# Kernel tuning notes

Hardware: AMD Instinct MI355X
Metric: run time of the kernel (lower is better)

Reference implementation:

```python
import jax, jax.numpy as jnp
import numpy as np
from jax import lax

V, D, P, C = 151936, 1024, 64, 28
B, S = 1, 1024
EPS = 1.1920929e-07  # torch.finfo(float32).eps, used by nn.RMSNorm(eps=None)


def setup_inputs() -> dict:
    key = jax.random.key(0)
    ks = jax.random.split(key, 10)
    return {
        "tokens": jax.random.randint(ks[0], (B, S), 0, V),
        "embed_table": jax.random.normal(ks[1], (V, D), jnp.float32) * 0.02,
        "plane_proj_w": jax.random.normal(ks[2], (C, 2 * P, D), jnp.float32) * (1.0 / np.sqrt(D)),
        "back_proj_w": jax.random.normal(ks[3], (C, D, 2 * P), jnp.float32) * 0.02,
        "base_angles": jax.random.normal(ks[4], (C, P), jnp.float32) * 0.1,
        "angle_gen_w": jax.random.normal(ks[5], (P, D), jnp.float32) * 0.01,
        "scales": jnp.ones((C, D), jnp.float32),
        "shifts": jnp.zeros((C, D), jnp.float32),
        "norm_w": jnp.ones((C, D), jnp.float32),
        "decay_param": jnp.float32(0.9),
        "gate_w": jax.random.normal(ks[6], (D, D), jnp.float32) * 0.02,
        "out_norm_w": jnp.ones((D,), jnp.float32),
        "lm_head_w": jax.random.normal(ks[7], (V, D), jnp.float32) * 0.02,
    }


def _rms_norm(v, w):
    return v * lax.rsqrt(jnp.mean(v * v, axis=-1, keepdims=True) + EPS) * w


def _causal_mix(x, decay_param, gate_w):
    # state_t = d*state_{t-1} + (1-d)*x_t, causal EMA over sequence
    d = jax.nn.sigmoid(decay_param)
    def step(s, xt):
        s = d * s + (1.0 - d) * xt
        return s, s
    _, ys = lax.scan(step, jnp.zeros(x.shape[::2], x.dtype)[0:0].sum(0) + jnp.zeros((x.shape[0], x.shape[2]), x.dtype), jnp.swapaxes(x, 0, 1))
    causal = jnp.swapaxes(ys, 0, 1)  # [B,S,D]
    return x + causal @ gate_w.T


def reference(tokens, embed_table, plane_proj_w, back_proj_w, base_angles,
              angle_gen_w, scales, shifts, norm_w, decay_param, gate_w,
              out_norm_w, lm_head_w):
    x = embed_table[tokens].astype(jnp.float32)  # [B,S,D]
    n_cycles = scales.shape[0]
    for i in range(n_cycles):
        # input-dependent angle offset (detached in the original)
        extra = x.mean(axis=1) @ angle_gen_w.T          # [B,P]
        angles = base_angles[i] + lax.stop_gradient(extra.mean(axis=0)) * 0.1
        if i % 4 == 0:
            x = _causal_mix(x, decay_param, gate_w)
        # learned-plane rotation
        proj = x @ plane_proj_w[i].T                     # [B,S,2P]
        n = proj.shape[-1] // 2
        a, b = proj[..., :n], proj[..., n:]
        ca, sa = jnp.cos(angles), jnp.sin(angles)
        rot = jnp.concatenate([a * ca - b * sa, a * sa + b * ca], axis=-1)
        x_rot = x + rot @ back_proj_w[i].T
        x_act = jax.nn.silu(x_rot * scales[i] + shifts[i])
        x = x + _rms_norm(x_act - x, norm_w[i])
    x = _rms_norm(x, out_norm_w)
    return x @ lm_head_w.T  # [B,S,V]
```

## Files before the change

### kernel.cpp

```cpp
#include <hip/hip_runtime.h>

typedef __attribute__((ext_vector_type(4))) float f32x4;
typedef __attribute__((ext_vector_type(8))) short bf16x8;
typedef unsigned short u16;
typedef unsigned int u32;
typedef __attribute__((ext_vector_type(4))) unsigned short u16x4;

#define EPS 1.1920929e-07f
#define S 1024
#define D 1024
#define NV 151936
#define NCYC 28
#define SMEM_BYTES 49152

__device__ __forceinline__ u16 f2bf(float f) {
  u32 u = __float_as_uint(f);
  return (u16)((u + 0x7fffu + ((u >> 16) & 1u)) >> 16);
}
__device__ __forceinline__ float bf2f(u16 h) {
  return __uint_as_float((u32)h << 16);
}
struct bfpair { u16 h, l; };
__device__ __forceinline__ bfpair split_bf(float v) {
  bfpair r;
  r.h = f2bf(v);
  r.l = f2bf(v - bf2f(r.h));
  return r;
}

__device__ __forceinline__ void gl16(const void* g, void* s) {
  __builtin_amdgcn_global_load_lds((const __attribute__((address_space(1))) u32*)g,
                                   (__attribute__((address_space(3))) u32*)s, 16, 0, 0);
}

__device__ __forceinline__ float block_sum256(float v, float* sbuf) {
  #pragma unroll
  for (int off = 32; off; off >>= 1) v += __shfl_down(v, off);
  int lane = threadIdx.x & 63, w = threadIdx.x >> 6;
  __syncthreads();
  if (lane == 0) sbuf[w] = v;
  __syncthreads();
  return sbuf[0] + sbuf[1] + sbuf[2] + sbuf[3];
}

__global__ void k_cvt(const float* __restrict__ src, u16* __restrict__ dst, size_t n4) {
  size_t i = (size_t)blockIdx.x * 256 + threadIdx.x;
  size_t stride = (size_t)gridDim.x * 256;
  for (; i < n4; i += stride) {
    f32x4 v = ((const f32x4*)src)[i];
    u16x4 o;
    #pragma unroll
    for (int e = 0; e < 4; ++e) o[e] = f2bf(v[e]);
    ((u16x4*)dst)[i] = o;
  }
}

__global__ void k_cvt2(const float* __restrict__ src, u16* __restrict__ dh,
                       u16* __restrict__ dl, size_t n4) {
  size_t i = (size_t)blockIdx.x * 256 + threadIdx.x;
  size_t stride = (size_t)gridDim.x * 256;
  for (; i < n4; i += stride) {
    f32x4 v = ((const f32x4*)src)[i];
    u16x4 oh, ol;
    #pragma unroll
    for (int e = 0; e < 4; ++e) { bfpair p = split_bf(v[e]); oh[e] = p.h; ol[e] = p.l; }
    ((u16x4*)dh)[i] = oh;
    ((u16x4*)dl)[i] = ol;
  }
}


__device__ void gather_phase(const int* tokens, const float* embed,
                             float* x, u16* xh, u16* xl, float* cp) {
  const int t = threadIdx.x;
  if (blockIdx.x >= 256) return;
  f32x4 creg = 0.f;
  for (int rr = 0; rr < 4; ++rr) {
    int s = blockIdx.x * 4 + rr;
    int tok = tokens[s];
    f32x4 v = ((const f32x4*)(embed + (size_t)tok * D))[t];
    u16x4 oh, ol;
    #pragma unroll
    for (int e = 0; e < 4; ++e) { bfpair p = split_bf(v[e]); oh[e] = p.h; ol[e] = p.l; }
    ((f32x4*)(x + (size_t)s * D))[t] = v;
    ((u16x4*)(xh + (size_t)s * D))[t] = oh;
    ((u16x4*)(xl + (size_t)s * D))[t] = ol;
    creg += v;
  }
  *(f32x4*)(cp + (size_t)blockIdx.x * D + t * 4) = creg;
}

template <bool CADD>
__device__ void gemm64_phase(char* smem, const u16* Ah_, const u16* Al_,
                             const u16* Bh_, const u16* Bl_, int K,
                             float* xout, u16* xho, u16* xlo, float* Cout, int G) {
  const int t = threadIdx.x;
  u16* Ash = (u16*)smem;
  u16* Asl = Ash + 4096;
  u16* Bsh = Asl + 4096;
  u16* Bsl = Bsh + 4096;
  const int wave = t >> 6, lane = t & 63;
  const int fr = lane & 15, kb = lane >> 4;
  const int sr = t >> 3, skc = (t & 7) << 3;
  const int sswz = skc ^ ((sr & 7) << 3);
  for (int tile = blockIdx.x; tile < 256; tile += G) {
    const int m0 = (tile >> 4) * 64, n0 = (tile & 15) * 64;
    f32x4 acc[4];
    #pragma unroll
    for (int j = 0; j < 4; ++j) acc[j] = 0.f;

    for (int k0 = 0; k0 < K; k0 += 64) {
      #pragma unroll
      for (int it = 0; it < 2; ++it) {
        int r = it * 32 + sr;
        size_t ga = (size_t)(m0 + r) * K + k0 + sswz;
        size_t gb = (size_t)(n0 + r) * K + k0 + sswz;
        int so = r * 64 + skc;
        gl16(Ah_ + ga, Ash + so);
        gl16(Al_ + ga, Asl + so);
        gl16(Bh_ + gb, Bsh + so);
        gl16(Bl_ + gb, Bsl + so);
      }
      __syncthreads();
      #pragma unroll
      for (int ks = 0; ks < 2; ++ks) {
        const int cphys = (ks * 32 + kb * 8) ^ ((fr & 7) << 3);
        int oa = (wave * 16 + fr) * 64 + cphys;
        bf16x8 ah = *(const bf16x8*)&Ash[oa];
        bf16x8 al = *(const bf16x8*)&Asl[oa];
        #pragma unroll
        for (int j = 0; j < 4; ++j) {
          int ob = (j * 16 + fr) * 64 + cphys;
          bf16x8 bh = *(const bf16x8*)&Bsh[ob];
          bf16x8 bl = *(const bf16x8*)&Bsl[ob];
          acc[j] = __builtin_amdgcn_mfma_f32_16x16x32_bf16(ah, bh, acc[j], 0, 0, 0);
          acc[j] = __builtin_amdgcn_mfma_f32_16x16x32_bf16(ah, bl, acc[j], 0, 0, 0);
          acc[j] = __builtin_amdgcn_mfma_f32_16x16x32_bf16(al, bh, acc[j], 0, 0, 0);
        }
      }
      __syncthreads();
    }
    #pragma unroll
    for (int j = 0; j < 4; ++j)
      #pragma unroll
      for (int rg = 0; rg < 4; ++rg) {
        int m = m0 + wave * 16 + kb * 4 + rg;
        int n = n0 + j * 16 + fr;
        if (CADD) {
          float v = xout[(size_t)m * D + n] + acc[j][rg];
          xout[(size_t)m * D + n] = v;
          bfpair p = split_bf(v);
          xho[(size_t)m * D + n] = p.h;
          xlo[(size_t)m * D + n] = p.l;
        } else {
          Cout[(size_t)m * D + n] = acc[j][rg];
        }
      }
  }
}

__device__ void causal_phase(char* smem, const float* x, u16* Rh, u16* Rl,
                             float dec, int G) {
  const int t = threadIdx.x;
  for (int tile = blockIdx.x; tile < 256; tile += G) {
    int s0 = (tile >> 4) * 64, d0 = (tile & 15) * 64;
    float (*tl)[64] = (float(*)[64])smem;
    for (int idx = t; idx < 159 * 64; idx += 256) {
      int rr = idx >> 6, c = idx & 63;
      int gs = s0 - 95 + rr;
      tl[rr][c] = (gs >= 0) ? x[(size_t)gs * D + d0 + c] : 0.f;
    }
    __syncthreads();
    int c = t & 63, r0 = t >> 6;
    for (int rr = r0; rr < 64; rr += 4) {
      float acc = 0.f, w = 1.f - dec;
      int base = rr + 95;
      #pragma unroll 8
      for (int j = 0; j < 96; ++j) { acc += w * tl[base - j][c]; w *= dec; }
      bfpair p = split_bf(acc);
      Rh[(size_t)(s0 + rr) * D + d0 + c] = p.h;
      Rl[(size_t)(s0 + rr) * D + d0 + c] = p.l;
    }
    __syncthreads();
  }
}

__device__ void proj_phase(char* smem, const u16* xh, const u16* xl,
                           const u16* Bh_, const u16* Bl_, float* pacc) {
  const int t = threadIdx.x;
  const int mt = blockIdx.x & 15, kq = blockIdx.x >> 4;
  const int m0 = mt * 64;
  const int k0 = kq * 64;
  u16* Ash = (u16*)smem;
  u16* Asl = Ash + 4096;
  u16* Bsh = Asl + 4096;
  u16* Bsl = Bsh + 8192;
  const int wave = t >> 6, lane = t & 63;
  const int fr = lane & 15, kb = lane >> 4;
  const int sr = t >> 3, skc = (t & 7) << 3;
  const int sswz = skc ^ ((sr & 7) << 3);
  f32x4 acc[8];
  #pragma unroll
  for (int j = 0; j < 8; ++j) acc[j] = 0.f;

  #pragma unroll
  for (int it = 0; it < 2; ++it) {
    int r = it * 32 + sr;
    size_t ga = (size_t)(m0 + r) * D + k0 + sswz;
    gl16(xh + ga, Ash + r * 64 + skc);
    gl16(xl + ga, Asl + r * 64 + skc);
  }
  #pragma unroll
  for (int it = 0; it < 4; ++it) {
    int r = it * 32 + sr;
    size_t gb = (size_t)r * D + k0 + sswz;
    gl16(Bh_ + gb, Bsh + r * 64 + skc);
    gl16(Bl_ + gb, Bsl + r * 64 + skc);
  }
  __syncthreads();
  #pragma unroll
  for (int ks = 0; ks < 2; ++ks) {
    const int cphys = (ks * 32 + kb * 8) ^ ((fr & 7) << 3);
    int oa = (wave * 16 + fr) * 64 + cphys;
    bf16x8 ah = *(const bf16x8*)&Ash[oa];
    bf16x8 al = *(const bf16x8*)&Asl[oa];
    #pragma unroll
    for (int j = 0; j < 8; ++j) {
      int ob = (j * 16 + fr) * 64 + cphys;
      bf16x8 bh = *(const bf16x8*)&Bsh[ob];
      bf16x8 bl = *(const bf16x8*)&Bsl[ob];
      acc[j] = __builtin_amdgcn_mfma_f32_16x16x32_bf16(ah, bh, acc[j], 0, 0, 0);
      acc[j] = __builtin_amdgcn_mfma_f32_16x16x32_bf16(ah, bl, acc[j], 0, 0, 0);
      acc[j] = __builtin_amdgcn_mfma_f32_16x16x32_bf16(al, bh, acc[j], 0, 0, 0);
    }
  }
  float* pb = pacc + (size_t)blockIdx.x * 64 * 128;
  #pragma unroll
  for (int j = 0; j < 8; ++j)
    #pragma unroll
    for (int rg = 0; rg < 4; ++rg) {
      int ml = wave * 16 + kb * 4 + rg;
      pb[ml * 128 + j * 16 + fr] = acc[j][rg];
    }
}

__device__ void angles_all(float* colsum, const float* cp, const float* agw,
                           const float* bang_i, float* trig) {
  const int t = threadIdx.x;
  f32x4 acc = 0.f;
  for (int b = 0; b < 256; ++b)
    acc += *(const f32x4*)(cp + (size_t)b * D + t * 4);
  *(f32x4*)&colsum[t * 4] = acc;
  __syncthreads();
  const int wave = t >> 6, lane = t & 63;
  for (int pp = 0; pp < 16; ++pp) {
    int p = wave * 16 + pp;
    float sum = 0.f;
    #pragma unroll
    for (int q = 0; q < 16; ++q) {
      int d = lane + q * 64;
      sum += colsum[d] * agw[p * D + d];
    }
    #pragma unroll
    for (int off = 32; off; off >>= 1) sum += __shfl_down(sum, off);
    if (lane == 0) {
      float ang = bang_i[p] + 0.1f * (sum * (1.f / (float)S));
      trig[p] = cosf(ang);
      trig[64 + p] = sinf(ang);
    }
  }
}

__device__ void epilogue_phase(float* sbuf, float* x, u16* xh, u16* xl,
                               const float* Rf, const float* scale,
                               const float* shift, const float* nw, float* cp) {
  const int t = threadIdx.x;
  if (blockIdx.x >= 256) return;
  f32x4 sc = *(const f32x4*)(scale + t * 4);
  f32x4 sh = *(const f32x4*)(shift + t * 4);
  f32x4 nwv = *(const f32x4*)(nw + t * 4);
  f32x4 creg = 0.f;
  for (int rr = 0; rr < 4; ++rr) {
    int s = blockIdx.x * 4 + rr;
    f32x4 xv = *(const f32x4*)(x + (size_t)s * D + t * 4);
    f32x4 rv = *(const f32x4*)(Rf + (size_t)s * D + t * 4);
    float y[4], ss = 0.f;
    #pragma unroll
    for (int c = 0; c < 4; ++c) {
      float xr = xv[c] + rv[c];
      float tt = xr * sc[c] + sh[c];
      float act = tt / (1.f + expf(-tt));
      y[c] = act - xv[c];
      ss += y[c] * y[c];
    }
    float total = block_sum256(ss, sbuf);
    float inv = rsqrtf(total * (1.f / (float)D) + EPS);
    f32x4 o;
    u16x4 oh, ol;
    #pragma unroll
    for (int c = 0; c < 4; ++c) {
      o[c] = xv[c] + y[c] * inv * nwv[c];
      bfpair p = split_bf(o[c]);
      oh[c] = p.h;
      ol[c] = p.l;
      creg[c] += o[c];
    }
    *(f32x4*)(x + (size_t)s * D + t * 4) = o;
    *(u16x4*)(xh + (size_t)s * D + t * 4) = oh;
    *(u16x4*)(xl + (size_t)s * D + t * 4) = ol;
  }
  *(f32x4*)(cp + (size_t)blockIdx.x * D + t * 4) = creg;
}

__device__ void outnorm_phase(float* sbuf, const float* x, const float* w, u16* xn) {
  const int t = threadIdx.x;
  if (blockIdx.x >= 256) return;
  for (int rr = 0; rr < 4; ++rr) {
    int s = blockIdx.x * 4 + rr;
    f32x4 xv = *(const f32x4*)(x + (size_t)s * D + t * 4);
    float total = block_sum256(xv[0]*xv[0] + xv[1]*xv[1] + xv[2]*xv[2] + xv[3]*xv[3], sbuf);
    float inv = rsqrtf(total * (1.f / (float)D) + EPS);
    f32x4 wv = *(const f32x4*)(w + t * 4);
    u16x4 o;
    #pragma unroll
    for (int c = 0; c < 4; ++c) o[c] = f2bf(xv[c] * inv * wv[c]);
    *(u16x4*)(xn + (size_t)s * D + t * 4) = o;
  }
}

__global__ __launch_bounds__(256) void fb_gather(const int* tokens, const float* embed,
                                                 float* x, u16* xh, u16* xl, float* cp) {
  gather_phase(tokens, embed, x, xh, xl, cp);
}
__global__ __launch_bounds__(256) void fb_causal(const float* x, u16* Rh, u16* Rl,
                                                 const float* decay) {
  __shared__ __align__(16) char sm[40704];
  causal_phase(sm, x, Rh, Rl, 1.f / (1.f + expf(-decay[0])), gridDim.x);
}
__global__ __launch_bounds__(256) void fb_gate(const u16* Rh, const u16* Rl,
                                               const u16* gh, const u16* gl,
                                               float* x, u16* xh, u16* xl) {
  __shared__ __align__(16) char sm[32768];
  gemm64_phase<true>(sm, Rh, Rl, gh, gl, 1024, x, xh, xl, nullptr, gridDim.x);
}
__global__ __launch_bounds__(256) void fb_proj(const u16* xh, const u16* xl,
                                               const u16* Wph, const u16* Wpl,
                                               const float* cp, const float* agw,
                                               const float* bang_i,
                                               float* pacc, float* trig) {
  __shared__ __align__(16) char sm[SMEM_BYTES];
  if (blockIdx.x < 256) proj_phase(sm, xh, xl, Wph, Wpl, pacc);
  else angles_all((float*)sm, cp, agw, bang_i, trig);
}

__global__ __launch_bounds__(256) void fb_back(const float* __restrict__ pacc,
                                               const float* __restrict__ trig,
                                               const u16* __restrict__ Bh_,
                                               const u16* __restrict__ Bl_,
                                               float* __restrict__ Rf) {
  __shared__ u16 Ash[64 * 128];
  __shared__ u16 Asl[64 * 128];
  __shared__ u16 Bsh[64 * 64];
  __shared__ u16 Bsl[64 * 64];
  const int t = threadIdx.x;
  const int tile = blockIdx.x;
  const int mt = tile >> 4;
  const int m0 = mt * 64, n0 = (tile & 15) * 64;
  const int wave = t >> 6, lane = t & 63;
  const int fr = lane & 15, kb = lane >> 4;
  const int sr = t >> 3, skc = (t & 7) << 3;
  const int sswz = skc ^ ((sr & 7) << 3);

  #pragma unroll
  for (int ri = 0; ri < 2; ++ri) {
    int r = ri * 32 + sr;
    int pdst = skc ^ ((r & 7) << 3);
    f32x4 a0 = 0.f, a1 = 0.f, b0 = 0.f, b1 = 0.f;
    #pragma unroll
    for (int kq = 0; kq < 16; ++kq) {
      const float* pk = pacc + ((size_t)(kq * 16 + mt) * 64 + r) * 128;
      a0 += *(const f32x4*)(pk + skc);
      a1 += *(const f32x4*)(pk + skc + 4);
      b0 += *(const f32x4*)(pk + 64 + skc);
      b1 += *(const f32x4*)(pk + 64 + skc + 4);
    }
    #pragma unroll
    for (int kh = 0; kh < 2; ++kh) {
      u16 hbuf[8], lbuf[8];
      #pragma unroll
      for (int j = 0; j < 8; ++j) {
        float av = (j < 4) ? a0[j & 3] : a1[j & 3];
        float bv = (j < 4) ? b0[j & 3] : b1[j & 3];
        float ca = trig[skc + j], sa = trig[64 + skc + j];
        float v = (kh == 0) ? (av * ca - bv * sa) : (av * sa + bv * ca);
        bfpair p = split_bf(v);
        hbuf[j] = p.h;
        lbuf[j] = p.l;
      }
      int so = r * 128 + kh * 64 + pdst;
      *(bf16x8*)&Ash[so] = *(bf16x8*)hbuf;
      *(bf16x8*)&Asl[so] = *(bf16x8*)lbuf;
    }
  }
  __syncthreads();

  f32x4 acc[4];
  #pragma unroll
  for (int j = 0; j < 4; ++j) acc[j] = 0.f;

  for (int kt = 0; kt < 2; ++kt) {
    int k0 = kt * 64;
    #pragma unroll
    for (int it = 0; it < 2; ++it) {
      int r = it * 32 + sr;
      size_t gb = (size_t)(n0 + r) * 128 + k0 + sswz;
      gl16(Bh_ + gb, Bsh + r * 64 + skc);
      gl16(Bl_ + gb, Bsl + r * 64 + skc);
    }
    __syncthreads();
    #pragma unroll
    for (int ks = 0; ks < 2; ++ks) {
      const int w = (ks * 32 + kb * 8) ^ ((fr & 7) << 3);
      int oa = (wave * 16 + fr) * 128 + k0 + w;
      bf16x8 ah = *(const bf16x8*)&Ash[oa];
      bf16x8 al = *(const bf16x8*)&Asl[oa];
      #pragma unroll
      for (int j = 0; j < 4; ++j) {
        int ob = (j * 16 + fr) * 64 + w;
        bf16x8 bh = *(const bf16x8*)&Bsh[ob];
        bf16x8 bl = *(const bf16x8*)&Bsl[ob];
        acc[j] = __builtin_amdgcn_mfma_f32_16x16x32_bf16(ah, bh, acc[j], 0, 0, 0);
        acc[j] = __builtin_amdgcn_mfma_f32_16x16x32_bf16(ah, bl, acc[j], 0, 0, 0);
        acc[j] = __builtin_amdgcn_mfma_f32_16x16x32_bf16(al, bh, acc[j], 0, 0, 0);
      }
    }
    __syncthreads();
  }
  #pragma unroll
  for (int j = 0; j < 4; ++j)
    #pragma unroll
    for (int rg = 0; rg < 4; ++rg) {
      int m = m0 + wave * 16 + kb * 4 + rg;
      int n = n0 + j * 16 + fr;
      Rf[(size_t)m * D + n] = acc[j][rg];
    }
}

__global__ __launch_bounds__(256) void fb_epi(float* x, u16* xh, u16* xl, const float* Rf,
                                              const float* scale, const float* shift,
                                              const float* nw, float* cp) {
  __shared__ float sbuf[4];
  epilogue_phase(sbuf, x, xh, xl, Rf, scale, shift, nw, cp);
}
__global__ __launch_bounds__(256) void fb_outnorm(const float* x, const float* w, u16* xn) {
  __shared__ float sbuf[4];
  outnorm_phase(sbuf, x, w, xn);
}

template <bool PRECONV>
__global__ __launch_bounds__(256) void k_lm(const u16* __restrict__ A,
                                            const void* __restrict__ Wsrc,
                                            float* __restrict__ out) {
  __shared__ u16 As[128 * 64];
  __shared__ u16 Bs[128 * 64];
  const int bid = blockIdx.x;
  const int lid = (bid & 7) * 1187 + (bid >> 3);
  const int m0 = (lid & 7) * 128;
  const int n0 = (lid >> 3) * 128;
  const int t = threadIdx.x;
  const int wave = t >> 6, lane = t & 63;
  const int wm = (wave >> 1) * 64, wn = (wave & 1) * 64;
  const int fr = lane & 15, kb = lane >> 4;
  const int sr = t >> 3, skc = (t & 7) << 3;
  const int sswz = skc ^ ((sr & 7) << 3);
  const u16* Wb16 = (const u16*)Wsrc;
  const float* Wf = (const float*)Wsrc;
  f32x4 acc[4][4];
  #pragma unroll
  for (int i = 0; i < 4; ++i)
    #pragma unroll
    for (int j = 0; j < 4; ++j) acc[i][j] = 0.f;

  for (int k0 = 0; k0 < D; k0 += 64) {
    #pragma unroll
    for (int it = 0; it < 4; ++it) {
      int r = it * 32 + sr;
      gl16(A + (size_t)(m0 + r) * D + k0 + sswz, As + r * 64 + skc);
    }
    if (PRECONV) {
      #pragma unroll
      for (int it = 0; it < 4; ++it) {
        int r = it * 32 + sr;
        gl16(Wb16 + (size_t)(n0 + r) * D + k0 + sswz, Bs + r * 64 + skc);
      }
    } else {
      #pragma unroll
      for (int it = 0; it < 4; ++it) {
        int r = it * 32 + sr;
        const float* src = Wf + (size_t)(n0 + r) * D + k0 + sswz;
        f32x4 v0 = *(const f32x4*)src;
        f32x4 v1 = *(const f32x4*)(src + 4);
        u16 h[8];
        #pragma unroll
        for (int e = 0; e < 4; ++e) { h[e] = f2bf(v0[e]); h[e + 4] = f2bf(v1[e]); }
        *(bf16x8*)&Bs[r * 64 + skc] = *(bf16x8*)h;
      }
    }
    __syncthreads();
    #pragma unroll
    for (int ks = 0; ks < 2; ++ks) {
      const int cphys = (ks * 32 + kb * 8) ^ ((fr & 7) << 3);
      bf16x8 a[4], b[4];
      #pragma unroll
      for (int i = 0; i < 4; ++i) a[i] = *(const bf16x8*)&As[(wm + i * 16 + fr) * 64 + cphys];
      #pragma unroll
      for (int j = 0; j < 4; ++j) b[j] = *(const bf16x8*)&Bs[(wn + j * 16 + fr) * 64 + cphys];
      #pragma unroll
      for (int i = 0; i < 4; ++i)
        #pragma unroll
        for (int j = 0; j < 4; ++j)
          acc[i][j] = __builtin_amdgcn_mfma_f32_16x16x32_bf16(a[i], b[j], acc[i][j], 0, 0, 0);
    }
    __syncthreads();
  }
  #pragma unroll
  for (int i = 0; i < 4; ++i)
    #pragma unroll
    for (int j = 0; j < 4; ++j)
      #pragma unroll
      for (int rg = 0; rg < 4; ++rg) {
        int m = m0 + wm + i * 16 + kb * 4 + rg;
        int n = n0 + wn + j * 16 + fr;
        out[(size_t)m * NV + n] = acc[i][j][rg];
      }
}

extern "C" void kernel_launch(void* const* d_in, const int* in_sizes, int n_in,
                              void* d_out, int out_size, void* d_ws, size_t ws_size,
                              hipStream_t stream) {
  const int* tokens = (const int*)d_in[0];
  const float* embed = (const float*)d_in[1];
  const float* Wp = (const float*)d_in[2];
  const float* Wb = (const float*)d_in[3];
  const float* bang = (const float*)d_in[4];
  const float* agw = (const float*)d_in[5];
  const float* scales = (const float*)d_in[6];
  const float* shifts = (const float*)d_in[7];
  const float* normw = (const float*)d_in[8];
  const float* decay = (const float*)d_in[9];
  const float* gatew = (const float*)d_in[10];
  const float* onorm = (const float*)d_in[11];
  const float* lmw = (const float*)d_in[12];
  float* out = (float*)d_out;

  char* ws = (char*)d_ws;
  const size_t MB = 1u << 20;
  float* x = (float*)ws;
  u16* xh = (u16*)(ws + 4 * MB);
  u16* xl = (u16*)(ws + 6 * MB);
  float* Rf = (float*)(ws + 8 * MB);
  u16* Rh = (u16*)(ws + 12 * MB);
  u16* Rl = (u16*)(ws + 14 * MB);
  float* trig = (float*)(ws + 16 * MB);
  float* cp = (float*)(ws + 17 * MB);
  u16* xn = (u16*)(ws + 20 * MB);
  u16* gate_h = (u16*)(ws + 22 * MB);
  u16* gate_l = (u16*)(ws + 24 * MB);
  u16* Wp_h = (u16*)(ws + 26 * MB);
  u16* Wp_l = (u16*)(ws + 33 * MB);
  u16* Wb_h = (u16*)(ws + 40 * MB);
  u16* Wb_l = (u16*)(ws + 47 * MB);
  float* pacc = (float*)(ws + 54 * MB);
  u16* lm_bf = (u16*)(ws + 62 * MB);

  const size_t lm_elems = (size_t)NV * D;
  bool preconv = ws_size >= 62 * MB + lm_elems * 2;

  k_cvt2<<<512, 256, 0, stream>>>(gatew, gate_h, gate_l, (size_t)D * D / 4);
  k_cvt2<<<1024, 256, 0, stream>>>(Wp, Wp_h, Wp_l, (size_t)NCYC * 128 * D / 4);
  k_cvt2<<<1024, 256, 0, stream>>>(Wb, Wb_h, Wb_l, (size_t)NCYC * 128 * D / 4);
  if (preconv) k_cvt<<<2048, 256, 0, stream>>>(lmw, lm_bf, lm_elems / 4);

  fb_gather<<<256, 256, 0, stream>>>(tokens, embed, x, xh, xl, cp);
  for (int i = 0; i < NCYC; ++i) {
    const u16* Wph = Wp_h + (size_t)i * 128 * D;
    const u16* Wpl = Wp_l + (size_t)i * 128 * D;
    const u16* Wbh = Wb_h + (size_t)i * 128 * D;
    const u16* Wbl = Wb_l + (size_t)i * 128 * D;
    if ((i & 3) == 0) {
      fb_causal<<<256, 256, 0, stream>>>(x, Rh, Rl, decay);
      fb_gate<<<256, 256, 0, stream>>>(Rh, Rl, gate_h, gate_l, x, xh, xl);
    }
    fb_proj<<<257, 256, 0, stream>>>(xh, xl, Wph, Wpl, cp, agw, bang + i * 64,
                                     pacc, trig);
    fb_back<<<256, 256, 0, stream>>>(pacc, trig, Wbh, Wbl, Rf);
    fb_epi<<<256, 256, 0, stream>>>(x, xh, xl, Rf, scales + i * D, shifts + i * D,
                                    normw + i * D, cp);
  }
  fb_outnorm<<<256, 256, 0, stream>>>(x, onorm, xn);

  if (preconv)
    k_lm<true><<<9496, 256, 0, stream>>>(xn, lm_bf, out);
  else
    k_lm<false><<<9496, 256, 0, stream>>>(xn, lmw, out);
}
```

Before: 2.822 ms.

## Overlap lm_head bf16 conversion with cycle kernels and double-buffer LM GEMM

The standalone conversion of the lm_head weights to bf16 is split into 84 chunks. Each chunk runs in extra blocks appended to the proj, back and epilogue launches of every cycle, so the conversion uses CUs those small 256-block kernels leave idle. The LM-head GEMM also gains double-buffered shared-memory staging, so the next K tile loads while the current one is computed. The cost is more shared memory per block, which may lower occupancy, and extra memory traffic competing with the latency-sensitive cycle kernels.

Measured after the change: 2.925 ms. 3.7% more time.

```diff
diff --git a/kernel.cpp b/kernel.cpp
--- a/kernel.cpp
+++ b/kernel.cpp
@@ -66,6 +66,24 @@
     for (int e = 0; e < 4; ++e) { bfpair p = split_bf(v[e]); oh[e] = p.h; ol[e] = p.l; }
     ((u16x4*)dh)[i] = oh;
     ((u16x4*)dl)[i] = ol;
+  }
+}
+
+__device__ void side_cvt(const float* __restrict__ src, u16* __restrict__ dst,
+                         int chunk, int blkbase) {
+  const size_t n4 = (size_t)NV * D / 4;
+  const size_t per = (n4 + (size_t)(NCYC * 3) - 1) / (size_t)(NCYC * 3);
+  size_t lo = (size_t)chunk * per;
+  size_t hi = lo + per;
+  if (hi > n4) hi = n4;
+  const size_t nb = (size_t)(gridDim.x - blkbase);
+  for (size_t i = lo + (size_t)(blockIdx.x - blkbase) * 256 + threadIdx.x; i < hi;
+       i += nb * 256) {
+    f32x4 v = ((const f32x4*)src)[i];
+    u16x4 o;
+    #pragma unroll
+    for (int e = 0; e < 4; ++e) o[e] = f2bf(v[e]);
+    ((u16x4*)dst)[i] = o;
   }
 }
 
@@ -275,7 +293,6 @@
                                const float* Rf, const float* scale,
                                const float* shift, const float* nw, float* cp) {
   const int t = threadIdx.x;
-  if (blockIdx.x >= 256) return;
   f32x4 sc = *(const f32x4*)(scale + t * 4);
   f32x4 sh = *(const f32x4*)(shift + t * 4);
   f32x4 nwv = *(const f32x4*)(nw + t * 4);
@@ -347,21 +364,25 @@
                                                const u16* Wph, const u16* Wpl,
                                                const float* cp, const float* agw,
                                                const float* bang_i,
-                                               float* pacc, float* trig) {
+                                               float* pacc, float* trig,
+                                               const float* lmw, u16* lm_bf, int chunk) {
   __shared__ __align__(16) char sm[SMEM_BYTES];
   if (blockIdx.x < 256) proj_phase(sm, xh, xl, Wph, Wpl, pacc);
-  else angles_all((float*)sm, cp, agw, bang_i, trig);
+  else if (blockIdx.x == 256) angles_all((float*)sm, cp, agw, bang_i, trig);
+  else side_cvt(lmw, lm_bf, chunk, 257);
 }
 
 __global__ __launch_bounds__(256) void fb_back(const float* __restrict__ pacc,
                                                const float* __restrict__ trig,
                                                const u16* __restrict__ Bh_,
                                                const u16* __restrict__ Bl_,
-                                               float* __restrict__ Rf) {
+                                               float* __restrict__ Rf,
+                                               const float* lmw, u16* lm_bf, int chunk) {
   __shared__ u16 Ash[64 * 128];
   __shared__ u16 Asl[64 * 128];
   __shared__ u16 Bsh[64 * 64];
   __shared__ u16 Bsl[64 * 64];
+  if (blockIdx.x >= 256) { side_cvt(lmw, lm_bf, chunk, 256); return; }
   const int t = threadIdx.x;
   const int tile = blockIdx.x;
   const int mt = tile >> 4;
@@ -448,9 +469,11 @@
 
 __global__ __launch_bounds__(256) void fb_epi(float* x, u16* xh, u16* xl, const float* Rf,
                                               const float* scale, const float* shift,
-                                              const float* nw, float* cp) {
+                                              const float* nw, float* cp,
+                                              const float* lmw, u16* lm_bf, int chunk) {
   __shared__ float sbuf[4];
-  epilogue_phase(sbuf, x, xh, xl, Rf, scale, shift, nw, cp);
+  if (blockIdx.x < 256) epilogue_phase(sbuf, x, xh, xl, Rf, scale, shift, nw, cp);
+  else side_cvt(lmw, lm_bf, chunk, 256);
 }
 __global__ __launch_bounds__(256) void fb_outnorm(const float* x, const float* w, u16* xn) {
   __shared__ float sbuf[4];
@@ -461,8 +484,8 @@
 __global__ __launch_bounds__(256) void k_lm(const u16* __restrict__ A,
                                             const void* __restrict__ Wsrc,
                                             float* __restrict__ out) {
-  __shared__ u16 As[128 * 64];
-  __shared__ u16 Bs[128 * 64];
+  __shared__ u16 As[2][128 * 64];
+  __shared__ u16 Bs[2][128 * 64];
   const int bid = blockIdx.x;
   const int lid = (bid & 7) * 1187 + (bid >> 3);
   const int m0 = (lid & 7) * 128;
@@ -481,17 +504,17 @@
     #pragma unroll
     for (int j = 0; j < 4; ++j) acc[i][j] = 0.f;
 
-  for (int k0 = 0; k0 < D; k0 += 64) {
+  auto stage = [&](int buf, int k0) {
     #pragma unroll
     for (int it = 0; it < 4; ++it) {
       int r = it * 32 + sr;
-      gl16(A + (size_t)(m0 + r) * D + k0 + sswz, As + r * 64 + skc);
+      gl16(A + (size_t)(m0 + r) * D + k0 + sswz, &As[buf][r * 64 + skc]);
     }
     if (PRECONV) {
       #pragma unroll
       for (int it = 0; it < 4; ++it) {
         int r = it * 32 + sr;
-        gl16(Wb16 + (size_t)(n0 + r) * D + k0 + sswz, Bs + r * 64 + skc);
+        gl16(Wb16 + (size_t)(n0 + r) * D + k0 + sswz, &Bs[buf][r * 64 + skc]);
       }
     } else {
       #pragma unroll
@@ -503,18 +526,24 @@
         u16 h[8];
         #pragma unroll
         for (int e = 0; e < 4; ++e) { h[e] = f2bf(v0[e]); h[e + 4] = f2bf(v1[e]); }
-        *(bf16x8*)&Bs[r * 64 + skc] = *(bf16x8*)h;
-      }
-    }
-    __syncthreads();
+        *(bf16x8*)&Bs[buf][r * 64 + skc] = *(bf16x8*)h;
+      }
+    }
+  };
+
+  stage(0, 0);
+  __syncthreads();
+  for (int kt = 0; kt < 16; ++kt) {
+    const int cur = kt & 1;
+    if (kt < 15) stage(cur ^ 1, (kt + 1) * 64);
     #pragma unroll
     for (int ks = 0; ks < 2; ++ks) {
       const int cphys = (ks * 32 + kb * 8) ^ ((fr & 7) << 3);
       bf16x8 a[4], b[4];
       #pragma unroll
-      for (int i = 0; i < 4; ++i) a[i] = *(const bf16x8*)&As[(wm + i * 16 + fr) * 64 + cphys];
-      #pragma unroll
-      for (int j = 0; j < 4; ++j) b[j] = *(const bf16x8*)&Bs[(wn + j * 16 + fr) * 64 + cphys];
+      for (int i = 0; i < 4; ++i) a[i] = *(const bf16x8*)&As[cur][(wm + i * 16 + fr) * 64 + cphys];
+      #pragma unroll
+      for (int j = 0; j < 4; ++j) b[j] = *(const bf16x8*)&Bs[cur][(wn + j * 16 + fr) * 64 + cphys];
       #pragma unroll
       for (int i = 0; i < 4; ++i)
         #pragma unroll
@@ -575,11 +604,14 @@
 
   const size_t lm_elems = (size_t)NV * D;
   bool preconv = ws_size >= 62 * MB + lm_elems * 2;
+  const float* side_src = preconv ? lmw : nullptr;
+  u16* side_dst = preconv ? lm_bf : nullptr;
+  const int gproj = preconv ? 385 : 257;
+  const int gside = preconv ? 384 : 256;
 
   k_cvt2<<<512, 256, 0, stream>>>(gatew, gate_h, gate_l, (size_t)D * D / 4);
   k_cvt2<<<1024, 256, 0, stream>>>(Wp, Wp_h, Wp_l, (size_t)NCYC * 128 * D / 4);
   k_cvt2<<<1024, 256, 0, stream>>>(Wb, Wb_h, Wb_l, (size_t)NCYC * 128 * D / 4);
-  if (preconv) k_cvt<<<2048, 256, 0, stream>>>(lmw, lm_bf, lm_elems / 4);
 
   fb_gather<<<256, 256, 0, stream>>>(tokens, embed, x, xh, xl, cp);
   for (int i = 0; i < NCYC; ++i) {
@@ -591,11 +623,12 @@
       fb_causal<<<256, 256, 0, stream>>>(x, Rh, Rl, decay);
       fb_gate<<<256, 256, 0, stream>>>(Rh, Rl, gate_h, gate_l, x, xh, xl);
     }
-    fb_proj<<<257, 256, 0, stream>>>(xh, xl, Wph, Wpl, cp, agw, bang + i * 64,
-                                     pacc, trig);
-    fb_back<<<256, 256, 0, stream>>>(pacc, trig, Wbh, Wbl, Rf);
-    fb_epi<<<256, 256, 0, stream>>>(x, xh, xl, Rf, scales + i * D, shifts + i * D,
-                                    normw + i * D, cp);
+    fb_proj<<<gproj, 256, 0, stream>>>(xh, xl, Wph, Wpl, cp, agw, bang + i * 64,
+                                       pacc, trig, side_src, side_dst, i * 3);
+    fb_back<<<gside, 256, 0, stream>>>(pacc, trig, Wbh, Wbl, Rf,
+                                       side_src, side_dst, i * 3 + 1);
+    fb_epi<<<gside, 256, 0, stream>>>(x, xh, xl, Rf, scales + i * D, shifts + i * D,
+                                      normw + i * D, cp, side_src, side_dst, i * 3 + 2);
   }
   fb_outnorm<<<256, 256, 0, stream>>>(x, onorm, xn);
 
```
